# Performance work log

Measured on AMD Instinct MI355X. Metric: run time of the kernel, lower is better.

The kernel has to match this reference:

```python
import jax, jax.numpy as jnp
import numpy as np

# Faithful translation of SIMPLE.imputate:
#   - first loop sets `last` to the LAST observed (mask<0.9) value in the row
#     (wrap-around initialization)
#   - second loop forward-fills: missing (mask>0.9) positions get `last`,
#     observed positions update `last`.
# Equivalent vectorized form: cummax of observed indices (forward-fill index),
# with leading missing positions falling back to the last observed index in the
# row, then a single gather.

def setup_inputs() -> dict:
    key = jax.random.key(0)
    k1, k2 = jax.random.split(key)
    B, N, D = 64, 4096, 128
    inp = jax.random.normal(k1, (B, N, D), dtype=jnp.float32)
    mask = jax.random.uniform(k2, (B, N), dtype=jnp.float32)  # >0.9 => missing
    return {"input": inp, "mask": mask}


def reference(input, mask):
    b, n, d = input.shape
    observed = mask < 0.9                       # [b, n] True where value is kept
    j = jnp.arange(n, dtype=jnp.int32)
    obs_idx = jnp.where(observed, j, jnp.int32(-1))           # [b, n]
    # index of most recent observed position <= j (inclusive cummax)
    ff_idx = jax.lax.associative_scan(jnp.maximum, obs_idx, axis=1)
    # wrap-around init: leading missing positions use the row's last observed idx
    last_overall = jnp.max(obs_idx, axis=1, keepdims=True)    # [b, 1]
    gather_idx = jnp.where(ff_idx < 0, last_overall, ff_idx)  # [b, n]
    gather_idx = jnp.maximum(gather_idx, 0)  # guard: row with no observed values
    out = jnp.take_along_axis(input, gather_idx[:, :, None], axis=1)  # [b, n, d]
    return out
```

## Files before the change

kernel.cpp:

```cpp
#include <hip/hip_runtime.h>


#define FF_N 4096
#define FF_D 128

typedef float f4 __attribute__((ext_vector_type(4)));

__global__ __launch_bounds__(256) void ffill_scan(const float* __restrict__ mask,
                                                  int* __restrict__ gidx) {
    const int b = blockIdx.x;
    const float* m = mask + (size_t)b * FF_N;
    int* g = gidx + (size_t)b * FF_N;
    const int tid  = threadIdx.x;
    const int base = tid * 16;

    float4 mv[4];
    const float4* m4 = reinterpret_cast<const float4*>(m + base);
#pragma unroll
    for (int k = 0; k < 4; ++k) mv[k] = m4[k];

    unsigned obsbits = 0;
    int segmax = -1;
#pragma unroll
    for (int k = 0; k < 4; ++k) {
        const float vals[4] = {mv[k].x, mv[k].y, mv[k].z, mv[k].w};
#pragma unroll
        for (int j = 0; j < 4; ++j) {
            const int idx = k * 4 + j;
            const bool o = vals[j] < 0.9f;
            obsbits |= (unsigned)o << idx;
            if (o) segmax = base + idx;
        }
    }

    const int lane = tid & 63;
    int incl = segmax;
#pragma unroll
    for (int off = 1; off < 64; off <<= 1) {
        const int t = __shfl_up(incl, off, 64);
        if (lane >= off) incl = max(incl, t);
    }

    __shared__ int wmax[4];
    if (lane == 63) wmax[tid >> 6] = incl;
    __syncthreads();
    const int wid = tid >> 6;
    int wpre = -1, total = -1;
#pragma unroll
    for (int w = 0; w < 4; ++w) {
        const int x = wmax[w];
        total = max(total, x);
        if (w < wid) wpre = max(wpre, x);
    }
    const int inclp  = __shfl_up(incl, 1, 64);
    const int prefix = max(wpre, (lane == 0) ? -1 : inclp);
    const int fallback = (total < 0) ? 0 : total;

    int last = prefix;
    int outv[16];
#pragma unroll
    for (int k = 0; k < 16; ++k) {
        if ((obsbits >> k) & 1u) last = base + k;
        outv[k] = (last < 0) ? fallback : last;
    }
    int4* g4 = reinterpret_cast<int4*>(g + base);
#pragma unroll
    for (int k = 0; k < 4; ++k)
        g4[k] = make_int4(outv[4 * k], outv[4 * k + 1], outv[4 * k + 2], outv[4 * k + 3]);
}

__global__ __launch_bounds__(256) void ffill_gather(const f4* __restrict__ in,
                                                    const int* __restrict__ gidx,
                                                    f4* __restrict__ out) {
    const int rowblk = blockIdx.x << 6;
    const int tid  = threadIdx.x;
    const int lane = tid & 31;
    const int rsub = tid >> 5;

    int gi[8];
#pragma unroll
    for (int i = 0; i < 8; ++i) gi[i] = gidx[rowblk + i * 8 + rsub];

    const int bbase = rowblk & ~(FF_N - 1);
    f4 v[8];
#pragma unroll
    for (int i = 0; i < 8; ++i)
        v[i] = in[(size_t)(bbase + gi[i]) * (FF_D / 4) + lane];

    const size_t ob = (size_t)rowblk * (FF_D / 4);
#pragma unroll
    for (int i = 0; i < 8; ++i)
        __builtin_nontemporal_store(v[i], &out[ob + i * 256 + tid]);
}

extern "C" void kernel_launch(void* const* d_in, const int* in_sizes, int n_in,
                              void* d_out, int out_size, void* d_ws, size_t ws_size,
                              hipStream_t stream) {
    const float* inp  = (const float*)d_in[0];
    const float* mask = (const float*)d_in[1];
    f4* out = (f4*)d_out;

    const int B = in_sizes[1] / FF_N;
    int* gidx = (int*)d_ws;

    ffill_scan<<<B, 256, 0, stream>>>(mask, gidx);
    ffill_gather<<<(B * FF_N) / 64, 256, 0, stream>>>((const f4*)inp, gidx, out);
}
```

Baseline: 236.3 us.

## Fuse mask scan and gather into one kernel with per-slice redundant scan

Merges the prefix-max scan kernel and the gather kernel into a single launch. Each block recomputes the row's scan over the full mask and keeps only its 128-row slice of indices in shared memory, then gathers 16 rows per thread group. This removes the second launch and the global index buffer round trip, at the cost of 32x redundant mask reads and scan work per batch row.

```diff
diff --git a/kernel.cpp b/kernel.cpp
--- a/kernel.cpp
+++ b/kernel.cpp
@@ -3,15 +3,22 @@
 
 #define FF_N 4096
 #define FF_D 128
+#define SLICES 32
+#define SLICE_N (FF_N / SLICES)
 
 typedef float f4 __attribute__((ext_vector_type(4)));
 
-__global__ __launch_bounds__(256) void ffill_scan(const float* __restrict__ mask,
-                                                  int* __restrict__ gidx) {
-    const int b = blockIdx.x;
+__global__ __launch_bounds__(256) void ffill_fused(const f4* __restrict__ in,
+                                                   const float* __restrict__ mask,
+                                                   f4* __restrict__ out) {
+    const int b   = blockIdx.x >> 5;
+    const int s   = blockIdx.x & 31;
+    const int tid = threadIdx.x;
+
+    __shared__ int wmax[4];
+    __shared__ int gslice[SLICE_N];
+
     const float* m = mask + (size_t)b * FF_N;
-    int* g = gidx + (size_t)b * FF_N;
-    const int tid  = threadIdx.x;
     const int base = tid * 16;
 
     float4 mv[4];
@@ -41,7 +48,6 @@
         if (lane >= off) incl = max(incl, t);
     }
 
-    __shared__ int wmax[4];
     if (lane == 63) wmax[tid >> 6] = incl;
     __syncthreads();
     const int wid = tid >> 6;
@@ -63,34 +69,32 @@
         if ((obsbits >> k) & 1u) last = base + k;
         outv[k] = (last < 0) ? fallback : last;
     }
-    int4* g4 = reinterpret_cast<int4*>(g + base);
+    if ((tid >> 3) == s) {
+        int4* g4 = reinterpret_cast<int4*>(&gslice[(tid & 7) * 16]);
 #pragma unroll
-    for (int k = 0; k < 4; ++k)
-        g4[k] = make_int4(outv[4 * k], outv[4 * k + 1], outv[4 * k + 2], outv[4 * k + 3]);
-}
+        for (int k = 0; k < 4; ++k)
+            g4[k] = make_int4(outv[4 * k], outv[4 * k + 1],
+                              outv[4 * k + 2], outv[4 * k + 3]);
+    }
+    __syncthreads();
 
-__global__ __launch_bounds__(256) void ffill_gather(const f4* __restrict__ in,
-                                                    const int* __restrict__ gidx,
-                                                    f4* __restrict__ out) {
-    const int rowblk = blockIdx.x << 6;
-    const int tid  = threadIdx.x;
-    const int lane = tid & 31;
+    const int l    = tid & 31;
     const int rsub = tid >> 5;
+    const f4* inb = in + (size_t)b * FF_N * (FF_D / 4);
 
-    int gi[8];
+    int gi[16];
 #pragma unroll
-    for (int i = 0; i < 8; ++i) gi[i] = gidx[rowblk + i * 8 + rsub];
+    for (int i = 0; i < 16; ++i) gi[i] = gslice[i * 8 + rsub];
 
-    const int bbase = rowblk & ~(FF_N - 1);
-    f4 v[8];
+    f4 v[16];
 #pragma unroll
-    for (int i = 0; i < 8; ++i)
-        v[i] = in[(size_t)(bbase + gi[i]) * (FF_D / 4) + lane];
+    for (int i = 0; i < 16; ++i)
+        v[i] = inb[(size_t)gi[i] * (FF_D / 4) + l];
 
-    const size_t ob = (size_t)rowblk * (FF_D / 4);
+    f4* outb = out + ((size_t)b * FF_N + (size_t)s * SLICE_N) * (FF_D / 4);
 #pragma unroll
-    for (int i = 0; i < 8; ++i)
-        __builtin_nontemporal_store(v[i], &out[ob + i * 256 + tid]);
+    for (int i = 0; i < 16; ++i)
+        __builtin_nontemporal_store(v[i], &outb[i * 256 + tid]);
 }
 
 extern "C" void kernel_launch(void* const* d_in, const int* in_sizes, int n_in,
@@ -101,8 +105,6 @@
     f4* out = (f4*)d_out;
 
     const int B = in_sizes[1] / FF_N;
-    int* gidx = (int*)d_ws;
-
-    ffill_scan<<<B, 256, 0, stream>>>(mask, gidx);
-    ffill_gather<<<(B * FF_N) / 64, 256, 0, stream>>>((const f4*)inp, gidx, out);
+    ffill_fused<<<B * SLICES, 256, 0, stream>>>(
+        (const f4*)inp, mask, out);
 }
```

New measurement: 238.4 us. Within noise of the previous version (+0.9%).
